# Kernel tuning notes

Hardware: AMD Instinct MI355X
Metric: run time of the kernel (lower is better)

Reference implementation:

```python
import jax, jax.numpy as jnp
import numpy as np

N_NODES = 100000


def gcn_conv(x, edge_index, W, b):
    """PyG GCNConv: h = D^{-1/2} (A + I) D^{-1/2} (x @ W) + b, edge weights = 1."""
    n = x.shape[0]
    loop = jnp.arange(n, dtype=edge_index.dtype)
    src = jnp.concatenate([edge_index[0], loop])  # row (source, message sender)
    dst = jnp.concatenate([edge_index[1], loop])  # col (target, aggregator)
    # symmetric normalization: deg over targets incl. self-loops
    deg = jnp.zeros((n,), dtype=x.dtype).at[dst].add(1.0)
    dinv = jnp.where(deg > 0, jax.lax.rsqrt(deg), 0.0)
    norm = dinv[src] * dinv[dst]  # [E+N]
    h = x @ W  # dense transform first (PyG order)
    msg = h[src] * norm[:, None]  # [E+N, hidden]
    out = jax.ops.segment_sum(msg, dst, num_segments=n)
    return out + b


def setup_inputs() -> dict:
    key = jax.random.key(0)
    k1, k2, k3, k4 = jax.random.split(key, 4)
    n, e, din, dh = N_NODES, 1600000, 128, 256
    x = jax.random.normal(k1, (n, din), dtype=jnp.float32)
    edge_index = jax.random.randint(k2, (2, e), 0, n, dtype=jnp.int32)
    # glorot-ish scaled weights
    W1 = jax.random.normal(k3, (din, dh), dtype=jnp.float32) * (1.0 / np.sqrt(din))
    W2 = jax.random.normal(k4, (dh, dh), dtype=jnp.float32) * (1.0 / np.sqrt(dh))
    b1 = jnp.zeros((dh,), dtype=jnp.float32)
    b2 = jnp.zeros((dh,), dtype=jnp.float32)
    return {"x": x, "edge_index": edge_index, "W1": W1, "b1": b1, "W2": W2, "b2": b2}


def reference(x, edge_index, W1, b1, W2, b2):
    h = jax.nn.relu(gcn_conv(x, edge_index, W1, b1))
    h = jax.nn.relu(gcn_conv(h, edge_index, W2, b2))
    return h
```

## Files before the change

### kernel.cpp

```cpp
#include <hip/hip_runtime.h>


__device__ __forceinline__ int rl(int v, int l) {
    return __builtin_amdgcn_readlane(v, l);
}
__device__ __forceinline__ float rlf(float v, int l) {
    return __int_as_float(__builtin_amdgcn_readlane(__float_as_int(v), l));
}

__global__ void count_kernel(const int* __restrict__ dst, int* __restrict__ cnt, int E) {
    int i = blockIdx.x * blockDim.x + threadIdx.x;
    if (i < E) atomicAdd(&cnt[dst[i]], 1);
}

__global__ __launch_bounds__(1024) void scan_kernel(const int* __restrict__ cnt,
                                                    int* __restrict__ roff,
                                                    float* __restrict__ dinv, int n) {
    __shared__ int wsum[16];
    __shared__ int carry_s, total_s;
    int tid = threadIdx.x;
    int lane = tid & 63, w = tid >> 6;
    if (tid == 0) carry_s = 0;
    __syncthreads();
    for (int base = 0; base < n; base += 1024) {
        int i = base + tid;
        int v = (i < n) ? cnt[i] : 0;
        if (i < n) dinv[i] = rsqrtf((float)v + 1.0f);
        int s = v;
#pragma unroll
        for (int d = 1; d < 64; d <<= 1) {
            int t = __shfl_up(s, d, 64);
            if (lane >= d) s += t;
        }
        if (lane == 63) wsum[w] = s;
        __syncthreads();
        if (w == 0) {
            int wv = (lane < 16) ? wsum[lane] : 0;
            int ss = wv;
#pragma unroll
            for (int d = 1; d < 16; d <<= 1) {
                int t = __shfl_up(ss, d, 64);
                if (lane >= d) ss += t;
            }
            if (lane < 16) wsum[lane] = ss - wv;
            if (lane == 15) total_s = ss;
        }
        __syncthreads();
        int carry = carry_s;
        if (i < n) roff[i] = carry + wsum[w] + (s - v);
        __syncthreads();
        if (tid == 0) carry_s += total_s;
        __syncthreads();
    }
}

__global__ void scatter_kernel(const int* __restrict__ src, const int* __restrict__ dst,
                               const int* __restrict__ roff, int* __restrict__ cur,
                               const float* __restrict__ dinv,
                               int* __restrict__ es, float* __restrict__ en, int E) {
    int i = blockIdx.x * blockDim.x + threadIdx.x;
    if (i < E) {
        int d = dst[i], s = src[i];
        int p = roff[d] + atomicAdd(&cur[d], 1);
        es[p] = s;
        en[p] = dinv[s] * dinv[d];
    }
}

template <int K, bool EPI>
__global__ __launch_bounds__(256) void sgemm_kernel(const float* __restrict__ A,
                                                    const float* __restrict__ B,
                                                    const float* __restrict__ bias,
                                                    float* __restrict__ C, int M) {
    __shared__ float As[8][128];
    __shared__ float Bs[8][128];
    int tid = threadIdx.x;
    int tx = tid & 15, ty = tid >> 4;
    int rowBase = blockIdx.x * 128;
    int colBase = blockIdx.y * 128;
    float acc[8][8] = {};
    int ar = rowBase + (tid >> 1);
    int ak = (tid & 1) * 4;
    int bk = tid >> 5;
    int bn = colBase + (tid & 31) * 4;

    for (int k0 = 0; k0 < K; k0 += 8) {
        float4 av = make_float4(0.f, 0.f, 0.f, 0.f);
        if (ar < M) av = *(const float4*)&A[(size_t)ar * K + k0 + ak];
        float4 bv = *(const float4*)&B[(size_t)(k0 + bk) * 256 + bn];
        __syncthreads();
        As[ak + 0][tid >> 1] = av.x;
        As[ak + 1][tid >> 1] = av.y;
        As[ak + 2][tid >> 1] = av.z;
        As[ak + 3][tid >> 1] = av.w;
        *(float4*)&Bs[bk][(tid & 31) * 4] = bv;
        __syncthreads();
#pragma unroll
        for (int kk = 0; kk < 8; ++kk) {
            float4 a0 = *(const float4*)&As[kk][ty * 8];
            float4 a1 = *(const float4*)&As[kk][ty * 8 + 4];
            float4 b0 = *(const float4*)&Bs[kk][tx * 8];
            float4 b1 = *(const float4*)&Bs[kk][tx * 8 + 4];
            float a[8] = {a0.x, a0.y, a0.z, a0.w, a1.x, a1.y, a1.z, a1.w};
            float b[8] = {b0.x, b0.y, b0.z, b0.w, b1.x, b1.y, b1.z, b1.w};
#pragma unroll
            for (int i = 0; i < 8; ++i)
#pragma unroll
                for (int j = 0; j < 8; ++j) acc[i][j] += a[i] * b[j];
        }
    }
    float bcol[8];
#pragma unroll
    for (int j = 0; j < 8; ++j) bcol[j] = EPI ? bias[colBase + tx * 8 + j] : 0.f;
#pragma unroll
    for (int i = 0; i < 8; ++i) {
        int r = rowBase + ty * 8 + i;
        if (r < M) {
            float o[8];
#pragma unroll
            for (int j = 0; j < 8; ++j)
                o[j] = EPI ? fmaxf(acc[i][j] + bcol[j], 0.f) : acc[i][j];
            *(float4*)&C[(size_t)r * 256 + colBase + tx * 8] =
                make_float4(o[0], o[1], o[2], o[3]);
            *(float4*)&C[(size_t)r * 256 + colBase + tx * 8 + 4] =
                make_float4(o[4], o[5], o[6], o[7]);
        }
    }
}

template <int WPN, int STRIDE_F2, bool EPI>
__global__ __launch_bounds__(256) void agg_kernel(const float2* __restrict__ H,
                                                  const int* __restrict__ roff,
                                                  const int* __restrict__ cnt,
                                                  const int* __restrict__ es,
                                                  const float* __restrict__ en,
                                                  const float* __restrict__ dinv,
                                                  const float* __restrict__ bias,
                                                  float2* __restrict__ out, int n) {
    int wv = threadIdx.x >> 6, lane = threadIdx.x & 63;
    int gw = blockIdx.x * 4 + wv;
    int node = (WPN == 1) ? gw : (gw >> 1);
    int half = (WPN == 1) ? 0 : (gw & 1);
    if (node >= n) return;
    int offF2 = half * 64 + lane;

    float di = dinv[node];
    float sn = di * di;
    float2 acc = H[(size_t)node * STRIDE_F2 + offF2];
    acc.x *= sn; acc.y *= sn;

    int beg = roff[node], m = cnt[node];
    for (int base = 0; base < m; base += 64) {
        int mm = min(64, m - base);
        int se = 0; float ne = 0.f;
        if (lane < mm) { se = es[beg + base + lane]; ne = en[beg + base + lane]; }
        int e = 0;
        for (; e + 8 <= mm; e += 8) {
            int s0 = rl(se, e + 0), s1 = rl(se, e + 1);
            int s2 = rl(se, e + 2), s3 = rl(se, e + 3);
            int s4 = rl(se, e + 4), s5 = rl(se, e + 5);
            int s6 = rl(se, e + 6), s7 = rl(se, e + 7);
            float n0 = rlf(ne, e + 0), n1 = rlf(ne, e + 1);
            float n2 = rlf(ne, e + 2), n3 = rlf(ne, e + 3);
            float n4 = rlf(ne, e + 4), n5 = rlf(ne, e + 5);
            float n6 = rlf(ne, e + 6), n7 = rlf(ne, e + 7);
            float2 h0 = H[(size_t)s0 * STRIDE_F2 + offF2];
            float2 h1 = H[(size_t)s1 * STRIDE_F2 + offF2];
            float2 h2 = H[(size_t)s2 * STRIDE_F2 + offF2];
            float2 h3 = H[(size_t)s3 * STRIDE_F2 + offF2];
            float2 h4 = H[(size_t)s4 * STRIDE_F2 + offF2];
            float2 h5 = H[(size_t)s5 * STRIDE_F2 + offF2];
            float2 h6 = H[(size_t)s6 * STRIDE_F2 + offF2];
            float2 h7 = H[(size_t)s7 * STRIDE_F2 + offF2];
            acc.x += h0.x * n0 + h1.x * n1 + h2.x * n2 + h3.x * n3;
            acc.y += h0.y * n0 + h1.y * n1 + h2.y * n2 + h3.y * n3;
            acc.x += h4.x * n4 + h5.x * n5 + h6.x * n6 + h7.x * n7;
            acc.y += h4.y * n4 + h5.y * n5 + h6.y * n6 + h7.y * n7;
        }
        for (; e < mm; ++e) {
            int s0 = rl(se, e);
            float n0 = rlf(ne, e);
            float2 h0 = H[(size_t)s0 * STRIDE_F2 + offF2];
            acc.x += h0.x * n0;
            acc.y += h0.y * n0;
        }
    }
    if (EPI) {
        float2 bb = ((const float2*)bias)[offF2];
        acc.x = fmaxf(acc.x + bb.x, 0.f);
        acc.y = fmaxf(acc.y + bb.y, 0.f);
    }
    out[(size_t)node * STRIDE_F2 + offF2] = acc;
}


extern "C" void kernel_launch(void* const* d_in, const int* in_sizes, int n_in,
                              void* d_out, int out_size, void* d_ws, size_t ws_size,
                              hipStream_t stream) {
    const float* x  = (const float*)d_in[0];
    const int*   ei = (const int*)d_in[1];
    const float* W1 = (const float*)d_in[2];
    const float* b1 = (const float*)d_in[3];
    const float* W2 = (const float*)d_in[4];
    const float* b2 = (const float*)d_in[5];
    float* out = (float*)d_out;

    const int n = in_sizes[0] / 128;
    const int E = in_sizes[1] / 2;
    const int* src = ei;
    const int* dst = ei + E;

    size_t off = 0;
    auto alloc = [&](size_t bytes) {
        void* p = (char*)d_ws + off;
        off += (bytes + 255) & ~(size_t)255;
        return p;
    };
    int*   cnt  = (int*)alloc((size_t)n * 4);
    int*   cur  = (int*)alloc((size_t)n * 4);
    int*   roff = (int*)alloc((size_t)n * 4);
    float* dinv = (float*)alloc((size_t)n * 4);
    int*   es   = (int*)alloc((size_t)E * 4);
    float* en   = (float*)alloc((size_t)E * 4);
    float* buf  = (float*)alloc((size_t)n * 256 * 4);
    (void)ws_size;

    hipMemsetAsync(cnt, 0, (size_t)(2 * n + 128) * 4, stream);
    count_kernel<<<(E + 255) / 256, 256, 0, stream>>>(dst, cnt, E);
    scan_kernel<<<1, 1024, 0, stream>>>(cnt, roff, dinv, n);
    scatter_kernel<<<(E + 255) / 256, 256, 0, stream>>>(src, dst, roff, cur, dinv, es, en, E);

    dim3 g1((n + 127) / 128, 2);
    agg_kernel<1, 64, false><<<(n + 3) / 4, 256, 0, stream>>>(
        (const float2*)x, roff, cnt, es, en, dinv, nullptr, (float2*)buf, n);
    sgemm_kernel<128, true><<<g1, 256, 0, stream>>>(buf, W1, b1, out, n);

    sgemm_kernel<256, false><<<g1, 256, 0, stream>>>(out, W2, nullptr, buf, n);
    agg_kernel<2, 128, true><<<(2 * n + 3) / 4, 256, 0, stream>>>(
        (const float2*)buf, roff, cnt, es, en, dinv, b2, (float2*)out, n);
}
```

Measured before the change: 1.032 ms.

## Store layer-2 transformed features as bf16 and pack edge src/norm into int2

```diff
diff --git a/kernel.cpp b/kernel.cpp
--- a/kernel.cpp
+++ b/kernel.cpp
@@ -1,12 +1,20 @@
 #include <hip/hip_runtime.h>
+
+typedef unsigned int uint32;
 
 
 __device__ __forceinline__ int rl(int v, int l) {
     return __builtin_amdgcn_readlane(v, l);
 }
-__device__ __forceinline__ float rlf(float v, int l) {
-    return __int_as_float(__builtin_amdgcn_readlane(__float_as_int(v), l));
-}
+__device__ __forceinline__ float rlf(int v, int l) {
+    return __int_as_float(__builtin_amdgcn_readlane(v, l));
+}
+__device__ __forceinline__ uint32 f2bf(float x) {
+    uint32 u = __float_as_uint(x);
+    return (u + 0x7fffu + ((u >> 16) & 1u)) >> 16;
+}
+__device__ __forceinline__ float bfLo(uint32 u) { return __uint_as_float(u << 16); }
+__device__ __forceinline__ float bfHi(uint32 u) { return __uint_as_float(u & 0xffff0000u); }
 
 __global__ void count_kernel(const int* __restrict__ dst, int* __restrict__ cnt, int E) {
     int i = blockIdx.x * blockDim.x + threadIdx.x;
@@ -57,17 +65,16 @@
 __global__ void scatter_kernel(const int* __restrict__ src, const int* __restrict__ dst,
                                const int* __restrict__ roff, int* __restrict__ cur,
                                const float* __restrict__ dinv,
-                               int* __restrict__ es, float* __restrict__ en, int E) {
+                               int2* __restrict__ ese, int E) {
     int i = blockIdx.x * blockDim.x + threadIdx.x;
     if (i < E) {
         int d = dst[i], s = src[i];
         int p = roff[d] + atomicAdd(&cur[d], 1);
-        es[p] = s;
-        en[p] = dinv[s] * dinv[d];
-    }
-}
-
-template <int K, bool EPI>
+        ese[p] = make_int2(s, __float_as_int(dinv[s] * dinv[d]));
+    }
+}
+
+template <int K, int OUT_MODE>
 __global__ __launch_bounds__(256) void sgemm_kernel(const float* __restrict__ A,
                                                     const float* __restrict__ B,
                                                     const float* __restrict__ bias,
@@ -111,86 +118,147 @@
     }
     float bcol[8];
 #pragma unroll
-    for (int j = 0; j < 8; ++j) bcol[j] = EPI ? bias[colBase + tx * 8 + j] : 0.f;
+    for (int j = 0; j < 8; ++j) bcol[j] = (OUT_MODE == 1) ? bias[colBase + tx * 8 + j] : 0.f;
 #pragma unroll
     for (int i = 0; i < 8; ++i) {
         int r = rowBase + ty * 8 + i;
         if (r < M) {
-            float o[8];
-#pragma unroll
-            for (int j = 0; j < 8; ++j)
-                o[j] = EPI ? fmaxf(acc[i][j] + bcol[j], 0.f) : acc[i][j];
-            *(float4*)&C[(size_t)r * 256 + colBase + tx * 8] =
-                make_float4(o[0], o[1], o[2], o[3]);
-            *(float4*)&C[(size_t)r * 256 + colBase + tx * 8 + 4] =
-                make_float4(o[4], o[5], o[6], o[7]);
-        }
-    }
-}
-
-template <int WPN, int STRIDE_F2, bool EPI>
-__global__ __launch_bounds__(256) void agg_kernel(const float2* __restrict__ H,
-                                                  const int* __restrict__ roff,
-                                                  const int* __restrict__ cnt,
-                                                  const int* __restrict__ es,
-                                                  const float* __restrict__ en,
-                                                  const float* __restrict__ dinv,
-                                                  const float* __restrict__ bias,
-                                                  float2* __restrict__ out, int n) {
+            if (OUT_MODE == 2) {
+                uint32* Cb = (uint32*)C;
+                uint4 pk;
+                pk.x = f2bf(acc[i][0]) | (f2bf(acc[i][1]) << 16);
+                pk.y = f2bf(acc[i][2]) | (f2bf(acc[i][3]) << 16);
+                pk.z = f2bf(acc[i][4]) | (f2bf(acc[i][5]) << 16);
+                pk.w = f2bf(acc[i][6]) | (f2bf(acc[i][7]) << 16);
+                *(uint4*)&Cb[(size_t)r * 128 + (colBase >> 1) + tx * 4] = pk;
+            } else {
+                float o[8];
+#pragma unroll
+                for (int j = 0; j < 8; ++j)
+                    o[j] = (OUT_MODE == 1) ? fmaxf(acc[i][j] + bcol[j], 0.f) : acc[i][j];
+                *(float4*)&C[(size_t)r * 256 + colBase + tx * 8] =
+                    make_float4(o[0], o[1], o[2], o[3]);
+                *(float4*)&C[(size_t)r * 256 + colBase + tx * 8 + 4] =
+                    make_float4(o[4], o[5], o[6], o[7]);
+            }
+        }
+    }
+}
+
+__global__ __launch_bounds__(256) void agg1_kernel(const float2* __restrict__ X,
+                                                   const int* __restrict__ roff,
+                                                   const int* __restrict__ cnt,
+                                                   const int2* __restrict__ ese,
+                                                   const float* __restrict__ dinv,
+                                                   float2* __restrict__ out, int n) {
     int wv = threadIdx.x >> 6, lane = threadIdx.x & 63;
-    int gw = blockIdx.x * 4 + wv;
-    int node = (WPN == 1) ? gw : (gw >> 1);
-    int half = (WPN == 1) ? 0 : (gw & 1);
+    int node = blockIdx.x * 4 + wv;
     if (node >= n) return;
-    int offF2 = half * 64 + lane;
 
     float di = dinv[node];
     float sn = di * di;
-    float2 acc = H[(size_t)node * STRIDE_F2 + offF2];
+    float2 acc = X[(size_t)node * 64 + lane];
     acc.x *= sn; acc.y *= sn;
 
     int beg = roff[node], m = cnt[node];
     for (int base = 0; base < m; base += 64) {
         int mm = min(64, m - base);
-        int se = 0; float ne = 0.f;
-        if (lane < mm) { se = es[beg + base + lane]; ne = en[beg + base + lane]; }
+        int2 ev = make_int2(0, 0);
+        if (lane < mm) ev = ese[beg + base + lane];
         int e = 0;
         for (; e + 8 <= mm; e += 8) {
-            int s0 = rl(se, e + 0), s1 = rl(se, e + 1);
-            int s2 = rl(se, e + 2), s3 = rl(se, e + 3);
-            int s4 = rl(se, e + 4), s5 = rl(se, e + 5);
-            int s6 = rl(se, e + 6), s7 = rl(se, e + 7);
-            float n0 = rlf(ne, e + 0), n1 = rlf(ne, e + 1);
-            float n2 = rlf(ne, e + 2), n3 = rlf(ne, e + 3);
-            float n4 = rlf(ne, e + 4), n5 = rlf(ne, e + 5);
-            float n6 = rlf(ne, e + 6), n7 = rlf(ne, e + 7);
-            float2 h0 = H[(size_t)s0 * STRIDE_F2 + offF2];
-            float2 h1 = H[(size_t)s1 * STRIDE_F2 + offF2];
-            float2 h2 = H[(size_t)s2 * STRIDE_F2 + offF2];
-            float2 h3 = H[(size_t)s3 * STRIDE_F2 + offF2];
-            float2 h4 = H[(size_t)s4 * STRIDE_F2 + offF2];
-            float2 h5 = H[(size_t)s5 * STRIDE_F2 + offF2];
-            float2 h6 = H[(size_t)s6 * STRIDE_F2 + offF2];
-            float2 h7 = H[(size_t)s7 * STRIDE_F2 + offF2];
+            int s0 = rl(ev.x, e + 0), s1 = rl(ev.x, e + 1);
+            int s2 = rl(ev.x, e + 2), s3 = rl(ev.x, e + 3);
+            int s4 = rl(ev.x, e + 4), s5 = rl(ev.x, e + 5);
+            int s6 = rl(ev.x, e + 6), s7 = rl(ev.x, e + 7);
+            float n0 = rlf(ev.y, e + 0), n1 = rlf(ev.y, e + 1);
+            float n2 = rlf(ev.y, e + 2), n3 = rlf(ev.y, e + 3);
+            float n4 = rlf(ev.y, e + 4), n5 = rlf(ev.y, e + 5);
+            float n6 = rlf(ev.y, e + 6), n7 = rlf(ev.y, e + 7);
+            float2 h0 = X[(size_t)s0 * 64 + lane];
+            float2 h1 = X[(size_t)s1 * 64 + lane];
+            float2 h2 = X[(size_t)s2 * 64 + lane];
+            float2 h3 = X[(size_t)s3 * 64 + lane];
+            float2 h4 = X[(size_t)s4 * 64 + lane];
+            float2 h5 = X[(size_t)s5 * 64 + lane];
+            float2 h6 = X[(size_t)s6 * 64 + lane];
+            float2 h7 = X[(size_t)s7 * 64 + lane];
             acc.x += h0.x * n0 + h1.x * n1 + h2.x * n2 + h3.x * n3;
             acc.y += h0.y * n0 + h1.y * n1 + h2.y * n2 + h3.y * n3;
             acc.x += h4.x * n4 + h5.x * n5 + h6.x * n6 + h7.x * n7;
             acc.y += h4.y * n4 + h5.y * n5 + h6.y * n6 + h7.y * n7;
         }
         for (; e < mm; ++e) {
-            int s0 = rl(se, e);
-            float n0 = rlf(ne, e);
-            float2 h0 = H[(size_t)s0 * STRIDE_F2 + offF2];
+            int s0 = rl(ev.x, e);
+            float n0 = rlf(ev.y, e);
+            float2 h0 = X[(size_t)s0 * 64 + lane];
             acc.x += h0.x * n0;
             acc.y += h0.y * n0;
         }
     }
-    if (EPI) {
-        float2 bb = ((const float2*)bias)[offF2];
-        acc.x = fmaxf(acc.x + bb.x, 0.f);
-        acc.y = fmaxf(acc.y + bb.y, 0.f);
-    }
-    out[(size_t)node * STRIDE_F2 + offF2] = acc;
+    out[(size_t)node * 64 + lane] = acc;
+}
+
+__global__ __launch_bounds__(256) void agg2_kernel(const uint32* __restrict__ Hbf,
+                                                   const int* __restrict__ roff,
+                                                   const int* __restrict__ cnt,
+                                                   const int2* __restrict__ ese,
+                                                   const float* __restrict__ dinv,
+                                                   const float* __restrict__ bias,
+                                                   float2* __restrict__ out, int n) {
+    int wv = threadIdx.x >> 6, lane = threadIdx.x & 63;
+    int gw = blockIdx.x * 4 + wv;
+    int node = gw >> 1, half = gw & 1;
+    if (node >= n) return;
+    int offU = half * 64 + lane;
+
+    float di = dinv[node];
+    float sn = di * di;
+    uint32 sg = Hbf[(size_t)node * 128 + offU];
+    float2 acc;
+    acc.x = bfLo(sg) * sn;
+    acc.y = bfHi(sg) * sn;
+
+    int beg = roff[node], m = cnt[node];
+    for (int base = 0; base < m; base += 64) {
+        int mm = min(64, m - base);
+        int2 ev = make_int2(0, 0);
+        if (lane < mm) ev = ese[beg + base + lane];
+        int e = 0;
+        for (; e + 8 <= mm; e += 8) {
+            int s0 = rl(ev.x, e + 0), s1 = rl(ev.x, e + 1);
+            int s2 = rl(ev.x, e + 2), s3 = rl(ev.x, e + 3);
+            int s4 = rl(ev.x, e + 4), s5 = rl(ev.x, e + 5);
+            int s6 = rl(ev.x, e + 6), s7 = rl(ev.x, e + 7);
+            float n0 = rlf(ev.y, e + 0), n1 = rlf(ev.y, e + 1);
+            float n2 = rlf(ev.y, e + 2), n3 = rlf(ev.y, e + 3);
+            float n4 = rlf(ev.y, e + 4), n5 = rlf(ev.y, e + 5);
+            float n6 = rlf(ev.y, e + 6), n7 = rlf(ev.y, e + 7);
+            uint32 g0 = Hbf[(size_t)s0 * 128 + offU];
+            uint32 g1 = Hbf[(size_t)s1 * 128 + offU];
+            uint32 g2 = Hbf[(size_t)s2 * 128 + offU];
+            uint32 g3 = Hbf[(size_t)s3 * 128 + offU];
+            uint32 g4 = Hbf[(size_t)s4 * 128 + offU];
+            uint32 g5 = Hbf[(size_t)s5 * 128 + offU];
+            uint32 g6 = Hbf[(size_t)s6 * 128 + offU];
+            uint32 g7 = Hbf[(size_t)s7 * 128 + offU];
+            acc.x += bfLo(g0) * n0 + bfLo(g1) * n1 + bfLo(g2) * n2 + bfLo(g3) * n3;
+            acc.y += bfHi(g0) * n0 + bfHi(g1) * n1 + bfHi(g2) * n2 + bfHi(g3) * n3;
+            acc.x += bfLo(g4) * n4 + bfLo(g5) * n5 + bfLo(g6) * n6 + bfLo(g7) * n7;
+            acc.y += bfHi(g4) * n4 + bfHi(g5) * n5 + bfHi(g6) * n6 + bfHi(g7) * n7;
+        }
+        for (; e < mm; ++e) {
+            int s0 = rl(ev.x, e);
+            float n0 = rlf(ev.y, e);
+            uint32 g0 = Hbf[(size_t)s0 * 128 + offU];
+            acc.x += bfLo(g0) * n0;
+            acc.y += bfHi(g0) * n0;
+        }
+    }
+    float2 bb = ((const float2*)bias)[offU];
+    acc.x = fmaxf(acc.x + bb.x, 0.f);
+    acc.y = fmaxf(acc.y + bb.y, 0.f);
+    out[(size_t)node * 128 + offU] = acc;
 }
 
 
@@ -220,22 +288,21 @@
     int*   cur  = (int*)alloc((size_t)n * 4);
     int*   roff = (int*)alloc((size_t)n * 4);
     float* dinv = (float*)alloc((size_t)n * 4);
-    int*   es   = (int*)alloc((size_t)E * 4);
-    float* en   = (float*)alloc((size_t)E * 4);
-    float* buf  = (float*)alloc((size_t)n * 256 * 4);
+    int2*  ese  = (int2*)alloc((size_t)E * 8);
+    float* buf  = (float*)alloc((size_t)n * 128 * 4);
     (void)ws_size;
 
     hipMemsetAsync(cnt, 0, (size_t)(2 * n + 128) * 4, stream);
     count_kernel<<<(E + 255) / 256, 256, 0, stream>>>(dst, cnt, E);
     scan_kernel<<<1, 1024, 0, stream>>>(cnt, roff, dinv, n);
-    scatter_kernel<<<(E + 255) / 256, 256, 0, stream>>>(src, dst, roff, cur, dinv, es, en, E);
+    scatter_kernel<<<(E + 255) / 256, 256, 0, stream>>>(src, dst, roff, cur, dinv, ese, E);
 
     dim3 g1((n + 127) / 128, 2);
-    agg_kernel<1, 64, false><<<(n + 3) / 4, 256, 0, stream>>>(
-        (const float2*)x, roff, cnt, es, en, dinv, nullptr, (float2*)buf, n);
-    sgemm_kernel<128, true><<<g1, 256, 0, stream>>>(buf, W1, b1, out, n);
-
-    sgemm_kernel<256, false><<<g1, 256, 0, stream>>>(out, W2, nullptr, buf, n);
-    agg_kernel<2, 128, true><<<(2 * n + 3) / 4, 256, 0, stream>>>(
-        (const float2*)buf, roff, cnt, es, en, dinv, b2, (float2*)out, n);
-}
+    agg1_kernel<<<(n + 3) / 4, 256, 0, stream>>>(
+        (const float2*)x, roff, cnt, ese, dinv, (float2*)buf, n);
+    sgemm_kernel<128, 1><<<g1, 256, 0, stream>>>(buf, W1, b1, out, n);
+
+    sgemm_kernel<256, 2><<<g1, 256, 0, stream>>>(out, W2, nullptr, buf, n);
+    agg2_kernel<<<(2 * n + 3) / 4, 256, 0, stream>>>(
+        (const uint32*)buf, roff, cnt, ese, dinv, b2, (float2*)out, n);
+}
```

Result: faster. 922.0 us (-10.7%).
